# Performance work log

Hardware: AMD Instinct MI355X
Metric: run time of the kernel (lower is better)

Reference implementation:

```python
import jax, jax.numpy as jnp
import numpy as np

HID = 128

def _gru_states(x, w_ih, w_hh, b_ih, b_hh):
    # x: [B,T,I]; w_ih: [3H,I]; w_hh: [3H,H]; biases: [3H]
    # Precompute input projections for all timesteps (one big GEMM).
    gi = jnp.einsum('bti,gi->tbg', x, w_ih) + b_ih  # [T,B,3H]
    B = x.shape[0]
    h0 = jnp.zeros((B, HID), dtype=x.dtype)

    def step(h, gi_t):
        gh = h @ w_hh.T + b_hh                      # [B,3H]
        i_r, i_z, i_n = jnp.split(gi_t, 3, axis=-1)
        h_r, h_z, h_n = jnp.split(gh, 3, axis=-1)
        r = jax.nn.sigmoid(i_r + h_r)
        z = jax.nn.sigmoid(i_z + h_z)
        n = jnp.tanh(i_n + r * h_n)
        h_new = (1.0 - z) * n + z * h
        return h_new, h_new

    _, states = jax.lax.scan(step, h0, gi)          # states: [T,B,H]
    return states


def setup_inputs() -> dict:
    key = jax.random.key(0)
    ks = jax.random.split(key, 7)
    B, T, I, H, E = 64, 2048, 128, HID, 64
    s_ih = 1.0 / np.sqrt(I)
    s_hh = 1.0 / np.sqrt(H)
    s_p = 1.0 / np.sqrt(H)
    return {
        'x': jax.random.normal(ks[0], (B, T, I), dtype=jnp.float32),
        'w_ih': jax.random.uniform(ks[1], (3 * H, I), jnp.float32, -s_ih, s_ih),
        'w_hh': jax.random.uniform(ks[2], (3 * H, H), jnp.float32, -s_hh, s_hh),
        'b_ih': jax.random.uniform(ks[3], (3 * H,), jnp.float32, -s_hh, s_hh),
        'b_hh': jax.random.uniform(ks[4], (3 * H,), jnp.float32, -s_hh, s_hh),
        'w_proj': jax.random.uniform(ks[5], (E, H), jnp.float32, -s_p, s_p),
        'b_proj': jax.random.uniform(ks[6], (E,), jnp.float32, -s_p, s_p),
    }


def reference(x, w_ih, w_hh, b_ih, b_hh, w_proj, b_proj):
    states = _gru_states(x, w_ih, w_hh, b_ih, b_hh)  # [T,B,H]
    pooled = states.mean(axis=0)                     # mean pooling over time -> [B,H]
    return pooled @ w_proj.T + b_proj                # [B,E]
```

## Files before the change

### kernel.cpp

```cpp
#include <hip/hip_runtime.h>
#include <math.h>

#define B_   64
#define T_   2048
#define HID_ 128
#define G3_  384
#define IN_  128
#define E_   64

#define TS_  128

typedef _Float16 f16x8 __attribute__((ext_vector_type(8)));
typedef float    f32x4 __attribute__((ext_vector_type(4)));

#define L2E  1.4426950408889634f
#define L2E2 2.8853900817779268f

#if __has_builtin(__builtin_amdgcn_exp2f)
#define EXP2(x) __builtin_amdgcn_exp2f(x)
#else
#define EXP2(x) __expf((x) * 0.6931471805599453f)
#endif

__device__ __forceinline__ float rcp_(float x) { return __builtin_amdgcn_rcpf(x); }

__device__ __forceinline__ f16x8 pack8_(float4 a, float4 b) {
    uint4 u;
    u.x = __builtin_bit_cast(unsigned, __builtin_amdgcn_cvt_pkrtz(a.x, a.y));
    u.y = __builtin_bit_cast(unsigned, __builtin_amdgcn_cvt_pkrtz(a.z, a.w));
    u.z = __builtin_bit_cast(unsigned, __builtin_amdgcn_cvt_pkrtz(b.x, b.y));
    u.w = __builtin_bit_cast(unsigned, __builtin_amdgcn_cvt_pkrtz(b.z, b.w));
    return __builtin_bit_cast(f16x8, u);
}

__device__ __forceinline__ void gemm_body(
    int g, int nTiles, int t0,
    const float* __restrict__ x, const float* __restrict__ w_ih,
    const float* __restrict__ b_ih, const float* __restrict__ b_hh,
    float* __restrict__ gi)
{
    const int tid = threadIdx.x;
    const int w   = tid >> 6;
    const int l   = tid & 63;
    const int ln  = l & 15;
    const int kq  = l >> 4;
    const int tt  = g % nTiles;
    const int b   = g / nTiles;
    const int tl_base = tt * TS_ + w * 16;

    const float* xb = x + ((size_t)b * T_ + (size_t)(t0 + tl_base)) * IN_;

    f16x8 afr[4];
    #pragma unroll
    for (int kc = 0; kc < 4; kc++) {
        const float* xr = xb + (size_t)ln * IN_ + kc * 32 + kq * 8;
        float4 p0 = *reinterpret_cast<const float4*>(xr);
        float4 p1 = *reinterpret_cast<const float4*>(xr + 4);
        afr[kc] = pack8_(p0, p1);
    }

    #pragma unroll
    for (int half = 0; half < 2; half++) {
        f32x4 acc[12];
        #pragma unroll
        for (int j = 0; j < 12; j++) acc[j] = (f32x4){0.f, 0.f, 0.f, 0.f};

        #pragma unroll
        for (int kc = 0; kc < 4; kc++) {
            #pragma unroll
            for (int j = 0; j < 12; j++) {
                const int nt = half * 12 + j;
                const float* wr = w_ih + (size_t)(nt * 16 + ln) * IN_ + kc * 32 + kq * 8;
                float4 q0 = *reinterpret_cast<const float4*>(wr);
                float4 q1 = *reinterpret_cast<const float4*>(wr + 4);
                const f16x8 bfr = pack8_(q0, q1);
                acc[j] = __builtin_amdgcn_mfma_f32_16x16x32_f16(afr[kc], bfr, acc[j], 0, 0, 0);
            }
        }

        #pragma unroll
        for (int j = 0; j < 12; j++) {
            const int col = half * 192 + j * 16 + ln;
            const float bias = b_ih[col] + (col < 256 ? b_hh[col] : 0.f);
            #pragma unroll
            for (int r = 0; r < 4; r++) {
                const size_t trow = (size_t)(tl_base + kq * 4 + r);
                gi[trow * (B_ * G3_) + (size_t)b * G3_ + col] = acc[j][r] + bias;
            }
        }
    }
}

#define REC_STEP(CUR, LD, TLOAD, PB)                                           \
  {                                                                            \
    const char* hb_ = (const char*)(&h2_sh[PB][0]) + kq * 16;                  \
    f16x8 af_[4];                                                              \
    af_[0] = __builtin_bit_cast(f16x8, *(const uint4*)(hb_));                  \
    af_[1] = __builtin_bit_cast(f16x8, *(const uint4*)(hb_ + 64));             \
    af_[2] = __builtin_bit_cast(f16x8, *(const uint4*)(hb_ + 128));            \
    af_[3] = __builtin_bit_cast(f16x8, *(const uint4*)(hb_ + 192));            \
    const float* gp_ = gib + (size_t)(TLOAD) * S;                              \
    LD[0] = gp_[cg]; LD[1] = gp_[cg + 128]; LD[2] = gp_[cg + 256];             \
    f32x4 a0_ = (f32x4){0.f, 0.f, 0.f, 0.f};                                   \
    f32x4 a1_ = (f32x4){0.f, 0.f, 0.f, 0.f};                                   \
    f32x4 a2_ = (f32x4){0.f, 0.f, 0.f, 0.f};                                   \
    a0_ = __builtin_amdgcn_mfma_f32_16x16x32_f16(af_[0], wf[0][0], a0_, 0, 0, 0); \
    a0_ = __builtin_amdgcn_mfma_f32_16x16x32_f16(af_[1], wf[0][1], a0_, 0, 0, 0); \
    a0_ = __builtin_amdgcn_mfma_f32_16x16x32_f16(af_[2], wf[0][2], a0_, 0, 0, 0); \
    a0_ = __builtin_amdgcn_mfma_f32_16x16x32_f16(af_[3], wf[0][3], a0_, 0, 0, 0); \
    a2_ = __builtin_amdgcn_mfma_f32_16x16x32_f16(af_[0], wf[2][0], a2_, 0, 0, 0); \
    a2_ = __builtin_amdgcn_mfma_f32_16x16x32_f16(af_[1], wf[2][1], a2_, 0, 0, 0); \
    a2_ = __builtin_amdgcn_mfma_f32_16x16x32_f16(af_[2], wf[2][2], a2_, 0, 0, 0); \
    a2_ = __builtin_amdgcn_mfma_f32_16x16x32_f16(af_[3], wf[2][3], a2_, 0, 0, 0); \
    const float yr_ = fmaf(CUR[0], L2E, a0_[0]);                               \
    const float r_  = rcp_(1.f + EXP2(-yr_));                                  \
    a1_ = __builtin_amdgcn_mfma_f32_16x16x32_f16(af_[0], wf[1][0], a1_, 0, 0, 0); \
    a1_ = __builtin_amdgcn_mfma_f32_16x16x32_f16(af_[1], wf[1][1], a1_, 0, 0, 0); \
    a1_ = __builtin_amdgcn_mfma_f32_16x16x32_f16(af_[2], wf[1][2], a1_, 0, 0, 0); \
    a1_ = __builtin_amdgcn_mfma_f32_16x16x32_f16(af_[3], wf[1][3], a1_, 0, 0, 0); \
    const float q_  = CUR[2] * L2E2;                                           \
    const float yn_ = fmaf(r_, a2_[0] + bh, q_);                               \
    const float u_  = rcp_(1.f + EXP2(yn_));                                   \
    const float n_  = fmaf(-2.f, u_, 1.f);                                     \
    const float yz_ = fmaf(CUR[1], L2E, a1_[0]);                               \
    const float z_  = rcp_(1.f + EXP2(-yz_));                                  \
    hj = n_ + z_ * (hj - n_);                                                  \
    hs += hj;                                                                  \
    if (kq == 0) h2_sh[(PB) ^ 1][cg] = (_Float16)hj;                           \
    __syncthreads();                                                           \
  }

__device__ __forceinline__ void rec_body(
    int b,
    const float* __restrict__ gi, const float* __restrict__ w_hh,
    const float* __restrict__ b_hh,
    const float* __restrict__ w_proj, const float* __restrict__ b_proj,
    float* __restrict__ out, float* __restrict__ state,
    int t0, int t1)
{
    const int tid  = threadIdx.x;
    const int w    = tid >> 6;
    const int lane = tid & 63;
    const int ln   = lane & 15;
    const int kq   = lane >> 4;
    const int wh   = w & 3;
    const int f    = w >> 2;
    const int cg   = 16 * wh + ln + 64 * f;
    const int nT   = t1 - t0;

    __shared__ _Float16 h2_sh[2][HID_];
    __shared__ float pooled[HID_];

    f16x8 wf[3][4];
    #pragma unroll
    for (int g = 0; g < 3; g++) {
        const float s = (g == 2) ? L2E2 : L2E;
        const float* wr = w_hh + (size_t)(128 * g + cg) * HID_;
        #pragma unroll
        for (int kc = 0; kc < 4; kc++) {
            const float* p = wr + kc * 32 + kq * 8;
            float4 q0 = *reinterpret_cast<const float4*>(p);
            float4 q1 = *reinterpret_cast<const float4*>(p + 4);
            q0.x *= s; q0.y *= s; q0.z *= s; q0.w *= s;
            q1.x *= s; q1.y *= s; q1.z *= s; q1.w *= s;
            wf[g][kc] = pack8_(q0, q1);
        }
    }
    const float bh = L2E2 * b_hh[256 + cg];

    float hj, hs;
    if (t0 == 0) { hj = hs = 0.f; }
    else {
        hj = state[b * HID_ + cg];
        hs = state[B_ * HID_ + b * HID_ + cg];
    }
    if (kq == 0) h2_sh[0][cg] = (_Float16)hj;
    __syncthreads();

    const float* gib = gi + (size_t)b * G3_;
    const size_t S = (size_t)B_ * G3_;

    float g0[3], g1[3], g2[3], g3[3];
    {
        const float* p0 = gib;
        const float* p1 = gib + S;
        g0[0] = p0[cg]; g0[1] = p0[cg + 128]; g0[2] = p0[cg + 256];
        g1[0] = p1[cg]; g1[1] = p1[cg + 128]; g1[2] = p1[cg + 256];
    }

    int pb = 0;
    const int nTm1 = nT - 1;
    for (int t = 0; t < nT; t += 4) {
        int t2 = t + 2 < nTm1 ? t + 2 : nTm1;
        int t3 = t + 3 < nTm1 ? t + 3 : nTm1;
        int t4 = t + 4 < nTm1 ? t + 4 : nTm1;
        int t5 = t + 5 < nTm1 ? t + 5 : nTm1;
        REC_STEP(g0, g2, t2, pb); pb ^= 1;
        REC_STEP(g1, g3, t3, pb); pb ^= 1;
        REC_STEP(g2, g0, t4, pb); pb ^= 1;
        REC_STEP(g3, g1, t5, pb); pb ^= 1;
    }

    if (t1 < T_) {
        if (kq == 0) {
            state[b * HID_ + cg]             = hj;
            state[B_ * HID_ + b * HID_ + cg] = hs;
        }
    } else {
        if (kq == 0) pooled[cg] = hs * (1.f / (float)T_);
        __syncthreads();
        if (tid < E_) {
            const float4* wpj = reinterpret_cast<const float4*>(w_proj + (size_t)tid * HID_);
            const float4* pp  = reinterpret_cast<const float4*>(pooled);
            float a0 = 0.f, a1 = 0.f, a2 = 0.f, a3 = 0.f;
            #pragma unroll
            for (int k = 0; k < 32; k++) {
                float4 wv = wpj[k]; float4 pv = pp[k];
                a0 = fmaf(wv.x, pv.x, a0);
                a1 = fmaf(wv.y, pv.y, a1);
                a2 = fmaf(wv.z, pv.z, a2);
                a3 = fmaf(wv.w, pv.w, a3);
            }
            out[b * E_ + tid] = (a0 + a1) + (a2 + a3) + b_proj[tid];
        }
    }
}

__global__ __launch_bounds__(512, 1)
void fused(const float* __restrict__ x, const float* __restrict__ w_ih,
           const float* __restrict__ b_ih, const float* __restrict__ w_hh,
           const float* __restrict__ b_hh,
           const float* __restrict__ w_proj, const float* __restrict__ b_proj,
           const float* __restrict__ gi_rec, float* __restrict__ gi_out,
           float* __restrict__ out, float* __restrict__ state,
           int trec0, int trec1, int tg0, int nRec, int nTiles)
{
    const int bid = (int)blockIdx.x;
    if (bid < nRec) {
        rec_body(bid, gi_rec, w_hh, b_hh, w_proj, b_proj, out, state, trec0, trec1);
    } else {
        gemm_body(bid - nRec, nTiles, tg0, x, w_ih, b_ih, b_hh, gi_out);
    }
}

extern "C" void kernel_launch(void* const* d_in, const int* in_sizes, int n_in,
                              void* d_out, int out_size, void* d_ws, size_t ws_size,
                              hipStream_t stream)
{
    const float* x      = (const float*)d_in[0];
    const float* w_ih   = (const float*)d_in[1];
    const float* w_hh   = (const float*)d_in[2];
    const float* b_ih   = (const float*)d_in[3];
    const float* b_hh   = (const float*)d_in[4];
    const float* w_proj = (const float*)d_in[5];
    const float* b_proj = (const float*)d_in[6];
    float* out = (float*)d_out;

    const size_t state_bytes = (size_t)2 * B_ * HID_ * sizeof(float);
    const size_t per_t = (size_t)B_ * G3_ * sizeof(float);

    const int NCK = 4;
    const int ck[NCK] = {128, 256, 640, 1024};
    const size_t buf0_rows = 640, buf1_rows = 1024;
    const size_t need = (buf0_rows + buf1_rows) * per_t + state_bytes;

    if (ws_size >= need) {
        float* buf[2] = { (float*)d_ws,
                          (float*)((char*)d_ws + buf0_rows * per_t) };
        float* state  = (float*)((char*)d_ws + (buf0_rows + buf1_rows) * per_t);
        int st[NCK + 1];
        st[0] = 0;
        for (int i = 0; i < NCK; i++) st[i + 1] = st[i] + ck[i];
        for (int i = 0; i <= NCK; i++) {
            const int rb = (i > 0)   ? B_ : 0;
            const int gb = (i < NCK) ? (ck[i] / TS_) * B_ : 0;
            const int trec0 = (i > 0) ? st[i - 1] : 0;
            const int trec1 = (i > 0) ? st[i]     : 0;
            const int tg0   = (i < NCK) ? st[i] : 0;
            const int nT    = (i < NCK) ? ck[i] / TS_ : 1;
            fused<<<dim3(rb + gb), dim3(512), 0, stream>>>(
                x, w_ih, b_ih, w_hh, b_hh, w_proj, b_proj,
                buf[(i + 1) & 1] , buf[i & 1],
                out, state, trec0, trec1, tg0, rb, nT);
        }
    } else {
        size_t avail = ws_size > state_bytes ? ws_size - state_bytes : 0;
        int cT = (int)(avail / per_t);
        if (cT > T_) cT = T_;
        cT &= ~(TS_ - 1);
        if (cT < TS_) cT = TS_;
        float* buf0  = (float*)d_ws;
        float* state = (float*)((char*)d_ws + (size_t)cT * per_t);
        for (int t0 = 0; t0 < T_; t0 += cT) {
            int t1 = t0 + cT; if (t1 > T_) t1 = T_;
            int nt = t1 - t0;
            fused<<<dim3((nt / TS_) * B_), dim3(512), 0, stream>>>(
                x, w_ih, b_ih, w_hh, b_hh, w_proj, b_proj,
                buf0, buf0, out, state, 0, 0, t0, 0, nt / TS_);
            fused<<<dim3(B_), dim3(512), 0, stream>>>(
                x, w_ih, b_ih, w_hh, b_hh, w_proj, b_proj,
                buf0, buf0, out, state, t0, t1, 0, B_, nt / TS_);
        }
    }
}
```

Before: 833.6 us.

## Split MFMA accumulator chains, cap GEMM blocks with persistent loop, rechunk pipeline

```diff
diff --git a/kernel.cpp b/kernel.cpp
--- a/kernel.cpp
+++ b/kernel.cpp
@@ -101,28 +101,27 @@
     af_[3] = __builtin_bit_cast(f16x8, *(const uint4*)(hb_ + 192));            \
     const float* gp_ = gib + (size_t)(TLOAD) * S;                              \
     LD[0] = gp_[cg]; LD[1] = gp_[cg + 128]; LD[2] = gp_[cg + 256];             \
-    f32x4 a0_ = (f32x4){0.f, 0.f, 0.f, 0.f};                                   \
-    f32x4 a1_ = (f32x4){0.f, 0.f, 0.f, 0.f};                                   \
-    f32x4 a2_ = (f32x4){0.f, 0.f, 0.f, 0.f};                                   \
-    a0_ = __builtin_amdgcn_mfma_f32_16x16x32_f16(af_[0], wf[0][0], a0_, 0, 0, 0); \
-    a0_ = __builtin_amdgcn_mfma_f32_16x16x32_f16(af_[1], wf[0][1], a0_, 0, 0, 0); \
-    a0_ = __builtin_amdgcn_mfma_f32_16x16x32_f16(af_[2], wf[0][2], a0_, 0, 0, 0); \
-    a0_ = __builtin_amdgcn_mfma_f32_16x16x32_f16(af_[3], wf[0][3], a0_, 0, 0, 0); \
-    a2_ = __builtin_amdgcn_mfma_f32_16x16x32_f16(af_[0], wf[2][0], a2_, 0, 0, 0); \
-    a2_ = __builtin_amdgcn_mfma_f32_16x16x32_f16(af_[1], wf[2][1], a2_, 0, 0, 0); \
-    a2_ = __builtin_amdgcn_mfma_f32_16x16x32_f16(af_[2], wf[2][2], a2_, 0, 0, 0); \
-    a2_ = __builtin_amdgcn_mfma_f32_16x16x32_f16(af_[3], wf[2][3], a2_, 0, 0, 0); \
-    const float yr_ = fmaf(CUR[0], L2E, a0_[0]);                               \
+    f32x4 zz_ = (f32x4){0.f, 0.f, 0.f, 0.f};                                   \
+    f32x4 a0A_ = zz_, a0B_ = zz_, a1A_ = zz_, a1B_ = zz_, a2A_ = zz_, a2B_ = zz_; \
+    a0A_ = __builtin_amdgcn_mfma_f32_16x16x32_f16(af_[0], wf[0][0], a0A_, 0, 0, 0); \
+    a0B_ = __builtin_amdgcn_mfma_f32_16x16x32_f16(af_[1], wf[0][1], a0B_, 0, 0, 0); \
+    a0A_ = __builtin_amdgcn_mfma_f32_16x16x32_f16(af_[2], wf[0][2], a0A_, 0, 0, 0); \
+    a0B_ = __builtin_amdgcn_mfma_f32_16x16x32_f16(af_[3], wf[0][3], a0B_, 0, 0, 0); \
+    a2A_ = __builtin_amdgcn_mfma_f32_16x16x32_f16(af_[0], wf[2][0], a2A_, 0, 0, 0); \
+    a2B_ = __builtin_amdgcn_mfma_f32_16x16x32_f16(af_[1], wf[2][1], a2B_, 0, 0, 0); \
+    a2A_ = __builtin_amdgcn_mfma_f32_16x16x32_f16(af_[2], wf[2][2], a2A_, 0, 0, 0); \
+    a2B_ = __builtin_amdgcn_mfma_f32_16x16x32_f16(af_[3], wf[2][3], a2B_, 0, 0, 0); \
+    const float yr_ = fmaf(CUR[0], L2E, a0A_[0] + a0B_[0]);                    \
     const float r_  = rcp_(1.f + EXP2(-yr_));                                  \
-    a1_ = __builtin_amdgcn_mfma_f32_16x16x32_f16(af_[0], wf[1][0], a1_, 0, 0, 0); \
-    a1_ = __builtin_amdgcn_mfma_f32_16x16x32_f16(af_[1], wf[1][1], a1_, 0, 0, 0); \
-    a1_ = __builtin_amdgcn_mfma_f32_16x16x32_f16(af_[2], wf[1][2], a1_, 0, 0, 0); \
-    a1_ = __builtin_amdgcn_mfma_f32_16x16x32_f16(af_[3], wf[1][3], a1_, 0, 0, 0); \
+    a1A_ = __builtin_amdgcn_mfma_f32_16x16x32_f16(af_[0], wf[1][0], a1A_, 0, 0, 0); \
+    a1B_ = __builtin_amdgcn_mfma_f32_16x16x32_f16(af_[1], wf[1][1], a1B_, 0, 0, 0); \
+    a1A_ = __builtin_amdgcn_mfma_f32_16x16x32_f16(af_[2], wf[1][2], a1A_, 0, 0, 0); \
+    a1B_ = __builtin_amdgcn_mfma_f32_16x16x32_f16(af_[3], wf[1][3], a1B_, 0, 0, 0); \
     const float q_  = CUR[2] * L2E2;                                           \
-    const float yn_ = fmaf(r_, a2_[0] + bh, q_);                               \
+    const float yn_ = fmaf(r_, a2A_[0] + a2B_[0] + bh, q_);                    \
     const float u_  = rcp_(1.f + EXP2(yn_));                                   \
     const float n_  = fmaf(-2.f, u_, 1.f);                                     \
-    const float yz_ = fmaf(CUR[1], L2E, a1_[0]);                               \
+    const float yz_ = fmaf(CUR[1], L2E, a1A_[0] + a1B_[0]);                    \
     const float z_  = rcp_(1.f + EXP2(-yz_));                                  \
     hj = n_ + z_ * (hj - n_);                                                  \
     hs += hj;                                                                  \
@@ -233,13 +232,15 @@
            const float* __restrict__ w_proj, const float* __restrict__ b_proj,
            const float* __restrict__ gi_rec, float* __restrict__ gi_out,
            float* __restrict__ out, float* __restrict__ state,
-           int trec0, int trec1, int tg0, int nRec, int nTiles)
+           int trec0, int trec1, int tg0, int nRec, int nTiles, int nJobs)
 {
     const int bid = (int)blockIdx.x;
     if (bid < nRec) {
         rec_body(bid, gi_rec, w_hh, b_hh, w_proj, b_proj, out, state, trec0, trec1);
     } else {
-        gemm_body(bid - nRec, nTiles, tg0, x, w_ih, b_ih, b_hh, gi_out);
+        const int np = (int)gridDim.x - nRec;
+        for (int j = bid - nRec; j < nJobs; j += np)
+            gemm_body(j, nTiles, tg0, x, w_ih, b_ih, b_hh, gi_out);
     }
 }
 
@@ -259,10 +260,11 @@
     const size_t state_bytes = (size_t)2 * B_ * HID_ * sizeof(float);
     const size_t per_t = (size_t)B_ * G3_ * sizeof(float);
 
-    const int NCK = 4;
-    const int ck[NCK] = {128, 256, 640, 1024};
-    const size_t buf0_rows = 640, buf1_rows = 1024;
+    const int NCK = 3;
+    const int ck[NCK] = {256, 512, 1280};
+    const size_t buf0_rows = 1280, buf1_rows = 512;
     const size_t need = (buf0_rows + buf1_rows) * per_t + state_bytes;
+    const int GMAX = 160;
 
     if (ws_size >= need) {
         float* buf[2] = { (float*)d_ws,
@@ -272,8 +274,9 @@
         st[0] = 0;
         for (int i = 0; i < NCK; i++) st[i + 1] = st[i] + ck[i];
         for (int i = 0; i <= NCK; i++) {
-            const int rb = (i > 0)   ? B_ : 0;
-            const int gb = (i < NCK) ? (ck[i] / TS_) * B_ : 0;
+            const int rb    = (i > 0)   ? B_ : 0;
+            const int jobs  = (i < NCK) ? (ck[i] / TS_) * B_ : 0;
+            const int gb    = jobs > GMAX ? GMAX : jobs;
             const int trec0 = (i > 0) ? st[i - 1] : 0;
             const int trec1 = (i > 0) ? st[i]     : 0;
             const int tg0   = (i < NCK) ? st[i] : 0;
@@ -281,7 +284,7 @@
             fused<<<dim3(rb + gb), dim3(512), 0, stream>>>(
                 x, w_ih, b_ih, w_hh, b_hh, w_proj, b_proj,
                 buf[(i + 1) & 1] , buf[i & 1],
-                out, state, trec0, trec1, tg0, rb, nT);
+                out, state, trec0, trec1, tg0, rb, nT, jobs);
         }
     } else {
         size_t avail = ws_size > state_bytes ? ws_size - state_bytes : 0;
@@ -294,12 +297,13 @@
         for (int t0 = 0; t0 < T_; t0 += cT) {
             int t1 = t0 + cT; if (t1 > T_) t1 = T_;
             int nt = t1 - t0;
-            fused<<<dim3((nt / TS_) * B_), dim3(512), 0, stream>>>(
+            const int jobs = (nt / TS_) * B_;
+            fused<<<dim3(jobs), dim3(512), 0, stream>>>(
                 x, w_ih, b_ih, w_hh, b_hh, w_proj, b_proj,
-                buf0, buf0, out, state, 0, 0, t0, 0, nt / TS_);
+                buf0, buf0, out, state, 0, 0, t0, 0, nt / TS_, jobs);
             fused<<<dim3(B_), dim3(512), 0, stream>>>(
                 x, w_ih, b_ih, w_hh, b_hh, w_proj, b_proj,
-                buf0, buf0, out, state, t0, t1, 0, B_, nt / TS_);
-        }
-    }
-}
+                buf0, buf0, out, state, t0, t1, 0, B_, nt / TS_, 0);
+        }
+    }
+}
```

New measurement: 889.5 us. 1.07x slower.

## Batch gi prefetch into 8-step register blocks and use uniform 512-step chunks

Applied to the files above, without the earlier changes.

```diff
diff --git a/kernel.cpp b/kernel.cpp
--- a/kernel.cpp
+++ b/kernel.cpp
@@ -9,6 +9,7 @@
 #define E_   64
 
 #define TS_  128
+#define CT_  512
 
 typedef _Float16 f16x8 __attribute__((ext_vector_type(8)));
 typedef float    f32x4 __attribute__((ext_vector_type(4)));
@@ -91,16 +92,14 @@
     }
 }
 
-#define REC_STEP(CUR, LD, TLOAD, PB)                                           \
+#define REC_CORE(CUR)                                                          \
   {                                                                            \
-    const char* hb_ = (const char*)(&h2_sh[PB][0]) + kq * 16;                  \
+    const char* hb_ = (const char*)(&h2_sh[pb][0]) + kq * 16;                  \
     f16x8 af_[4];                                                              \
     af_[0] = __builtin_bit_cast(f16x8, *(const uint4*)(hb_));                  \
     af_[1] = __builtin_bit_cast(f16x8, *(const uint4*)(hb_ + 64));             \
     af_[2] = __builtin_bit_cast(f16x8, *(const uint4*)(hb_ + 128));            \
     af_[3] = __builtin_bit_cast(f16x8, *(const uint4*)(hb_ + 192));            \
-    const float* gp_ = gib + (size_t)(TLOAD) * S;                              \
-    LD[0] = gp_[cg]; LD[1] = gp_[cg + 128]; LD[2] = gp_[cg + 256];             \
     f32x4 a0_ = (f32x4){0.f, 0.f, 0.f, 0.f};                                   \
     f32x4 a1_ = (f32x4){0.f, 0.f, 0.f, 0.f};                                   \
     f32x4 a2_ = (f32x4){0.f, 0.f, 0.f, 0.f};                                   \
@@ -126,9 +125,22 @@
     const float z_  = rcp_(1.f + EXP2(-yz_));                                  \
     hj = n_ + z_ * (hj - n_);                                                  \
     hs += hj;                                                                  \
-    if (kq == 0) h2_sh[(PB) ^ 1][cg] = (_Float16)hj;                           \
+    if (kq == 0) h2_sh[pb ^ 1][cg] = (_Float16)hj;                             \
     __syncthreads();                                                           \
+    pb ^= 1;                                                                   \
   }
+
+#define LOAD8(DST, TB)                                                         \
+  _Pragma("unroll")                                                            \
+  for (int j = 0; j < 8; j++) {                                                \
+    int rr_ = (TB) + j; rr_ = rr_ < nTm1 ? rr_ : nTm1;                         \
+    const float* gp_ = gib + (size_t)rr_ * S;                                  \
+    DST[j][0] = gp_[cg]; DST[j][1] = gp_[cg + 128]; DST[j][2] = gp_[cg + 256]; \
+  }
+
+#define STEP8(SRC)                                                             \
+  _Pragma("unroll")                                                            \
+  for (int j = 0; j < 8; j++) { REC_CORE(SRC[j]); }
 
 __device__ __forceinline__ void rec_body(
     int b,
@@ -174,31 +186,23 @@
         hj = state[b * HID_ + cg];
         hs = state[B_ * HID_ + b * HID_ + cg];
     }
+
+    const float* gib = gi + (size_t)b * G3_;
+    const size_t S = (size_t)B_ * G3_;
+    const int nTm1 = nT - 1;
+
+    float gA[8][3], gB[8][3];
+    LOAD8(gA, 0);
+
     if (kq == 0) h2_sh[0][cg] = (_Float16)hj;
     __syncthreads();
 
-    const float* gib = gi + (size_t)b * G3_;
-    const size_t S = (size_t)B_ * G3_;
-
-    float g0[3], g1[3], g2[3], g3[3];
-    {
-        const float* p0 = gib;
-        const float* p1 = gib + S;
-        g0[0] = p0[cg]; g0[1] = p0[cg + 128]; g0[2] = p0[cg + 256];
-        g1[0] = p1[cg]; g1[1] = p1[cg + 128]; g1[2] = p1[cg + 256];
-    }
-
     int pb = 0;
-    const int nTm1 = nT - 1;
-    for (int t = 0; t < nT; t += 4) {
-        int t2 = t + 2 < nTm1 ? t + 2 : nTm1;
-        int t3 = t + 3 < nTm1 ? t + 3 : nTm1;
-        int t4 = t + 4 < nTm1 ? t + 4 : nTm1;
-        int t5 = t + 5 < nTm1 ? t + 5 : nTm1;
-        REC_STEP(g0, g2, t2, pb); pb ^= 1;
-        REC_STEP(g1, g3, t3, pb); pb ^= 1;
-        REC_STEP(g2, g0, t4, pb); pb ^= 1;
-        REC_STEP(g3, g1, t5, pb); pb ^= 1;
+    for (int tb = 0; tb < nT; tb += 16) {
+        LOAD8(gB, tb + 8);
+        STEP8(gA);
+        LOAD8(gA, tb + 16);
+        STEP8(gB);
     }
 
     if (t1 < T_) {
@@ -259,29 +263,20 @@
     const size_t state_bytes = (size_t)2 * B_ * HID_ * sizeof(float);
     const size_t per_t = (size_t)B_ * G3_ * sizeof(float);
 
-    const int NCK = 4;
-    const int ck[NCK] = {128, 256, 640, 1024};
-    const size_t buf0_rows = 640, buf1_rows = 1024;
-    const size_t need = (buf0_rows + buf1_rows) * per_t + state_bytes;
-
-    if (ws_size >= need) {
+    if (ws_size >= 2 * (size_t)CT_ * per_t + state_bytes) {
         float* buf[2] = { (float*)d_ws,
-                          (float*)((char*)d_ws + buf0_rows * per_t) };
-        float* state  = (float*)((char*)d_ws + (buf0_rows + buf1_rows) * per_t);
-        int st[NCK + 1];
-        st[0] = 0;
-        for (int i = 0; i < NCK; i++) st[i + 1] = st[i] + ck[i];
-        for (int i = 0; i <= NCK; i++) {
-            const int rb = (i > 0)   ? B_ : 0;
-            const int gb = (i < NCK) ? (ck[i] / TS_) * B_ : 0;
-            const int trec0 = (i > 0) ? st[i - 1] : 0;
-            const int trec1 = (i > 0) ? st[i]     : 0;
-            const int tg0   = (i < NCK) ? st[i] : 0;
-            const int nT    = (i < NCK) ? ck[i] / TS_ : 1;
+                          (float*)((char*)d_ws + (size_t)CT_ * per_t) };
+        float* state  = (float*)((char*)d_ws + 2 * (size_t)CT_ * per_t);
+        const int nTiles = CT_ / TS_;
+        const int nC = T_ / CT_;
+        for (int i = 0; i <= nC; i++) {
+            const int rb = (i > 0)  ? B_ : 0;
+            const int gb = (i < nC) ? nTiles * B_ : 0;
             fused<<<dim3(rb + gb), dim3(512), 0, stream>>>(
                 x, w_ih, b_ih, w_hh, b_hh, w_proj, b_proj,
                 buf[(i + 1) & 1] , buf[i & 1],
-                out, state, trec0, trec1, tg0, rb, nT);
+                out, state,
+                (i - 1) * CT_, i * CT_, i * CT_, rb, nTiles);
         }
     } else {
         size_t avail = ws_size > state_bytes ? ws_size - state_bytes : 0;
```

Result: no change. 833.7 us (+0.0%).
